# Performance work log

Measured on AMD Instinct MI355X. Metric: run time of the kernel, lower is better.

## Reference

```python
import jax, jax.numpy as jnp
import numpy as np

ANG = 5  # angRes; n = ANG*ANG
EPS = 1e-12  # torch F.normalize eps

def _l2norm(x, axis):
    n = jnp.sqrt(jnp.sum(x * x, axis=axis, keepdims=True))
    return x / jnp.maximum(n, EPS)

def setup_inputs() -> dict:
    key = jax.random.key(0)
    kq, kk, kv = jax.random.split(key, 3)
    shape = (16, 16, 25, 16, 128)  # b c n h w
    return {
        "token_q": jax.random.normal(kq, shape, dtype=jnp.float32),
        "token_k": jax.random.normal(kk, shape, dtype=jnp.float32),
        "token_v": jax.random.normal(kv, shape, dtype=jnp.float32),
    }

def reference(token_q, token_k, token_v):
    b, c, n, h, w = token_q.shape
    u = v = ANG
    buffer = token_v

    def to_q(x):  # b c (u v) h w -> b (c h) (w u v)
        return x.reshape(b, c, u, v, h, w).transpose(0, 1, 4, 5, 2, 3).reshape(b, c * h, w * u * v)

    def to_k(x):  # b c (u v) h w -> b (w u v) (c h)
        return x.reshape(b, c, u, v, h, w).transpose(0, 5, 2, 3, 1, 4).reshape(b, w * u * v, c * h)

    unfold_q = _l2norm(to_q(token_q), axis=-1)      # [b, ch, wuv]
    unfold_k = _l2norm(to_k(token_k), axis=-2)      # [b, wuv, ch]
    unfold_v = to_q(token_v)                        # [b, ch, wuv]

    att = jnp.einsum('bts,bsr->btr', unfold_q, unfold_k)  # [b, ch, ch]
    size = c * h
    causal = jnp.tril(jnp.ones((size, size), dtype=bool))
    att = jnp.where(causal, att, jnp.float32(-1e15))
    att = jax.nn.softmax(att, axis=-1)

    out = jnp.einsum('btr,brs->bts', att, unfold_v)  # [b, ch, wuv]
    # b (c h) (w u v) -> b c (u v) h w
    out = out.reshape(b, c, h, w, u, v).transpose(0, 1, 4, 5, 2, 3).reshape(b, c, n, h, w)
    return out + buffer
```

## Files before the change

kernel.cpp:

```cpp
#include <hip/hip_runtime.h>
#include <math.h>

#define SB 819200
#define SC 51200
#define SN 2048
#define CH 256
#define NW 3200
#define NPARTS 5
#define PARTLEN 640
#define SPART 1048576

typedef __bf16 bf16x8 __attribute__((ext_vector_type(8)));
typedef __bf16 bf16x4 __attribute__((ext_vector_type(4)));
typedef float  f32x4  __attribute__((ext_vector_type(4)));

__device__ __forceinline__ bf16x8 cvt8(float4 a, float4 b) {
    bf16x8 r;
    r[0] = (__bf16)a.x; r[1] = (__bf16)a.y; r[2] = (__bf16)a.z; r[3] = (__bf16)a.w;
    r[4] = (__bf16)b.x; r[5] = (__bf16)b.y; r[6] = (__bf16)b.z; r[7] = (__bf16)b.w;
    return r;
}

__global__ __launch_bounds__(256) void norms_kernel(const float* __restrict__ q,
                                                    const float* __restrict__ k,
                                                    float* __restrict__ inv_nq,
                                                    float* __restrict__ inv_nk) {
    const int wave = threadIdx.x >> 6;
    const int lane = threadIdx.x & 63;
    const int row = blockIdx.x * 4 + wave;
    const int b = row >> 8;
    const int t = row & 255;
    const size_t base = (size_t)b * SB + (size_t)(t >> 4) * SC +
                        (size_t)(t & 15) * 128 + lane * 2;
    float sq = 0.f, sk = 0.f;
#pragma unroll
    for (int nch = 0; nch < 25; nch++) {
        const float2 a = *(const float2*)(q + base + (size_t)nch * SN);
        const float2 c = *(const float2*)(k + base + (size_t)nch * SN);
        sq += a.x * a.x + a.y * a.y;
        sk += c.x * c.x + c.y * c.y;
    }
#pragma unroll
    for (int off = 32; off; off >>= 1) {
        sq += __shfl_xor(sq, off, 64);
        sk += __shfl_xor(sk, off, 64);
    }
    if (lane == 0) {
        inv_nq[row] = 1.0f / fmaxf(sqrtf(sq), 1e-12f);
        inv_nk[row] = 1.0f / fmaxf(sqrtf(sk), 1e-12f);
    }
}

__global__ __launch_bounds__(256, 2) void gemm1_kernel(const float* __restrict__ q,
                                                       const float* __restrict__ k,
                                                       float* __restrict__ Sp) {
    __shared__ alignas(16) __bf16 As[128 * 72];
    __shared__ alignas(16) __bf16 Bs[128 * 72];

    const int tid = threadIdx.x;
    const int b = blockIdx.z;
    const int part = blockIdx.y;
    const int tile = blockIdx.x;
    const int tm = (tile + 1) >> 1;
    const int tn = tile >> 1;

    const int lane = tid & 63;
    const int wave = tid >> 6;
    const int wm = wave >> 1;
    const int wn = wave & 1;

    const int srow = tid >> 1;
    const int scol = (tid & 1) * 32;
    const int ta = tm * 128 + srow;
    const int rb = tn * 128 + srow;
    const float* qrow = q + (size_t)b * SB + (size_t)(ta >> 4) * SC + (size_t)(ta & 15) * 128;
    const float* krow = k + (size_t)b * SB + (size_t)(rb >> 4) * SC + (size_t)(rb & 15) * 128;

    f32x4 acc[4][4] = {};
    bool live[4][4];
#pragma unroll
    for (int mi = 0; mi < 4; mi++)
#pragma unroll
        for (int ni = 0; ni < 4; ni++)
            live[mi][ni] = (tn * 128 + wn * 64 + ni * 16) <= (tm * 128 + wm * 64 + mi * 16);

    for (int ch = 0; ch < 10; ch++) {
        const int kg = part * PARTLEN + ch * 64;
        const size_t koff = (size_t)(kg >> 7) * SN + (kg & 127) + scol;

        float4 av[8], bv[8];
#pragma unroll
        for (int j = 0; j < 8; j++) {
            av[j] = *(const float4*)(qrow + koff + j * 4);
            bv[j] = *(const float4*)(krow + koff + j * 4);
        }
        __syncthreads();
#pragma unroll
        for (int j = 0; j < 4; j++) {
            *(bf16x8*)&As[srow * 72 + scol + j * 8] = cvt8(av[2 * j], av[2 * j + 1]);
            *(bf16x8*)&Bs[srow * 72 + scol + j * 8] = cvt8(bv[2 * j], bv[2 * j + 1]);
        }
        __syncthreads();
#pragma unroll
        for (int ks = 0; ks < 2; ks++) {
            const int ko = ks * 32 + (lane >> 4) * 8;
            bf16x8 af[4], bf[4];
#pragma unroll
            for (int mi = 0; mi < 4; mi++)
                af[mi] = *(const bf16x8*)&As[(wm * 64 + mi * 16 + (lane & 15)) * 72 + ko];
#pragma unroll
            for (int ni = 0; ni < 4; ni++)
                bf[ni] = *(const bf16x8*)&Bs[(wn * 64 + ni * 16 + (lane & 15)) * 72 + ko];
#pragma unroll
            for (int mi = 0; mi < 4; mi++)
#pragma unroll
                for (int ni = 0; ni < 4; ni++)
                    if (live[mi][ni])
                        acc[mi][ni] = __builtin_amdgcn_mfma_f32_16x16x32_bf16(
                            af[mi], bf[ni], acc[mi][ni], 0, 0, 0);
        }
    }

    float* o = Sp + (size_t)part * SPART + (size_t)b * 65536;
#pragma unroll
    for (int mi = 0; mi < 4; mi++)
#pragma unroll
        for (int ni = 0; ni < 4; ni++) {
            if (!live[mi][ni]) continue;
            const int r = tn * 128 + wn * 64 + ni * 16 + (lane & 15);
#pragma unroll
            for (int j = 0; j < 4; j++) {
                const int t = tm * 128 + wm * 64 + mi * 16 + (lane >> 4) * 4 + j;
                o[(size_t)t * 256 + r] = acc[mi][ni][j];
            }
        }
}

__global__ __launch_bounds__(256) void softmax_kernel(const float* __restrict__ Sp,
                                                      const float* __restrict__ inv_nq,
                                                      const float* __restrict__ inv_nk,
                                                      __bf16* __restrict__ P) {
    const int wave = threadIdx.x >> 6;
    const int lane = threadIdx.x & 63;
    const int t = blockIdx.x * 4 + wave;
    const int b = blockIdx.y;
    const size_t rowbase = ((size_t)b * 256 + t) * 256;
    const int r0 = lane * 4;

    float4 s4 = {0.f, 0.f, 0.f, 0.f};
#pragma unroll
    for (int p = 0; p < NPARTS; p++) {
        const float4 x = *(const float4*)(Sp + (size_t)p * SPART + rowbase + r0);
        s4.x += x.x; s4.y += x.y; s4.z += x.z; s4.w += x.w;
    }
    const float qn = inv_nq[b * 256 + t];
    const float4 kn = *(const float4*)(inv_nk + b * 256 + r0);

    float val[4] = {s4.x * qn * kn.x, s4.y * qn * kn.y,
                    s4.z * qn * kn.z, s4.w * qn * kn.w};
    float m = -1e30f;
#pragma unroll
    for (int j = 0; j < 4; j++) {
        if (r0 + j > t) val[j] = -1e30f;
        m = fmaxf(m, val[j]);
    }
#pragma unroll
    for (int off = 32; off; off >>= 1) m = fmaxf(m, __shfl_xor(m, off, 64));

    float e[4], sum = 0.f;
#pragma unroll
    for (int j = 0; j < 4; j++) {
        e[j] = (r0 + j <= t) ? expf(val[j] - m) : 0.f;
        sum += e[j];
    }
#pragma unroll
    for (int off = 32; off; off >>= 1) sum += __shfl_xor(sum, off, 64);

    const float inv = 1.0f / sum;
    bf16x4 o;
    o[0] = (__bf16)(e[0] * inv);
    o[1] = (__bf16)(e[1] * inv);
    o[2] = (__bf16)(e[2] * inv);
    o[3] = (__bf16)(e[3] * inv);
    *(bf16x4*)(P + rowbase + r0) = o;
}

__global__ __launch_bounds__(256, 4) void gemm2_kernel(const __bf16* __restrict__ P,
                                                       const float* __restrict__ v,
                                                       float* __restrict__ out) {
    __shared__ alignas(16) char smem[36864];
    __bf16* Ps = (__bf16*)smem;
    __bf16* Vs = (__bf16*)(smem + 18432);
    float* Es = (float*)smem;

    const int tid = threadIdx.x;
    const int b = blockIdx.z;
    const int tt = blockIdx.y;
    const int n = blockIdx.x;

    const int lane = tid & 63;
    const int wave = tid >> 6;
    const int wm = wave >> 1;
    const int wn = wave & 1;

    const int prow = tid >> 1;
    const int pcol = (tid & 1) * 32;
    const __bf16* Prow = P + ((size_t)b * 256 + tt * 128 + prow) * 256;

    const int vu = tid & 7;
    const int vr = tid >> 3;
    const float* vbase = v + (size_t)b * SB + (size_t)n * SN;

    f32x4 acc[4][4] = {};

    for (int kc = 0; kc < 4; kc++) {
        bf16x8 p4[4];
#pragma unroll
        for (int j = 0; j < 4; j++)
            p4[j] = *(const bf16x8*)(Prow + kc * 64 + pcol + j * 8);

        float4 vv[2][4];
#pragma unroll
        for (int g = 0; g < 2; g++) {
            const int rg = kc * 64 + vr + g * 32;
            const float* vrow = vbase + (size_t)(rg >> 4) * SC + (size_t)(rg & 15) * 128;
#pragma unroll
            for (int jj = 0; jj < 4; jj++)
                vv[g][jj] = *(const float4*)(vrow + vu * 16 + jj * 4);
        }
        __syncthreads();
#pragma unroll
        for (int j = 0; j < 4; j++)
            *(bf16x8*)&Ps[prow * 72 + pcol + j * 8] = p4[j];
#pragma unroll
        for (int g = 0; g < 2; g++) {
            const int rl = vr + g * 32;
            const int rsw = rl ^ (vu << 3);
#pragma unroll
            for (int jj = 0; jj < 4; jj++) {
                const float* f = (const float*)&vv[g][jj];
#pragma unroll
                for (int e = 0; e < 4; e++) {
                    const int s = vu * 16 + jj * 4 + e;
                    Vs[s * 72 + rsw] = (__bf16)f[e];
                }
            }
        }
        __syncthreads();
#pragma unroll
        for (int ks = 0; ks < 2; ks++) {
            const int ko = ks * 32 + (lane >> 4) * 8;
            bf16x8 af[4], bf[4];
#pragma unroll
            for (int mi = 0; mi < 4; mi++)
                af[mi] = *(const bf16x8*)&Ps[(wm * 64 + mi * 16 + (lane & 15)) * 72 + ko];
#pragma unroll
            for (int ni = 0; ni < 4; ni++) {
                const int s0 = wn * 64 + ni * 16;
                const int sw = ((s0 >> 4) & 7) << 3;
                bf[ni] = *(const bf16x8*)&Vs[(s0 + (lane & 15)) * 72 + (ko ^ sw)];
            }
#pragma unroll
            for (int mi = 0; mi < 4; mi++)
#pragma unroll
                for (int ni = 0; ni < 4; ni++)
                    acc[mi][ni] = __builtin_amdgcn_mfma_f32_16x16x32_bf16(
                        af[mi], bf[ni], acc[mi][ni], 0, 0, 0);
        }
        __syncthreads();
    }

    for (int half = 0; half < 2; half++) {
        if (half == 1) __syncthreads();
        if (wm == half) {
#pragma unroll
            for (int mi = 0; mi < 4; mi++)
#pragma unroll
                for (int ni = 0; ni < 4; ni++)
#pragma unroll
                    for (int j = 0; j < 4; j++) {
                        const int trow = mi * 16 + (lane >> 4) * 4 + j;
                        const int wcol = wn * 64 + ni * 16 + (lane & 15);
                        Es[trow * 132 + wcol] = acc[mi][ni][j];
                    }
        }
        __syncthreads();
#pragma unroll
        for (int it = 0; it < 8; it++) {
            const int tl = it * 8 + (tid >> 5);
            const int w4 = (tid & 31) * 4;
            const int t = tt * 128 + half * 64 + tl;
            const size_t a = (size_t)b * SB + (size_t)(t >> 4) * SC + (size_t)n * SN +
                             (size_t)(t & 15) * 128 + w4;
            float4 r4 = *(const float4*)&Es[tl * 132 + w4];
            const float4 buf = *(const float4*)(v + a);
            r4.x += buf.x; r4.y += buf.y; r4.z += buf.z; r4.w += buf.w;
            *(float4*)(out + a) = r4;
        }
    }
}

extern "C" void kernel_launch(void* const* d_in, const int* in_sizes, int n_in,
                              void* d_out, int out_size, void* d_ws, size_t ws_size,
                              hipStream_t stream) {
    const float* q = (const float*)d_in[0];
    const float* k = (const float*)d_in[1];
    const float* v = (const float*)d_in[2];
    float* out = (float*)d_out;

    float* ws = (float*)d_ws;
    float* inv_nq = ws;
    float* inv_nk = ws + 4096;
    __bf16* P = (__bf16*)(ws + 8192);

    float* Spart = out;

    norms_kernel<<<dim3(1024), dim3(256), 0, stream>>>(q, k, inv_nq, inv_nk);
    gemm1_kernel<<<dim3(3, NPARTS, 16), dim3(256), 0, stream>>>(q, k, Spart);
    softmax_kernel<<<dim3(64, 16), dim3(256), 0, stream>>>(Spart, inv_nq, inv_nk, P);
    gemm2_kernel<<<dim3(25, 2, 16), dim3(256), 0, stream>>>(P, v, out);
}
```

Baseline: 246.6 us.

## Fuse norms into gemm1 launch and split gemm2 into narrower W tiles

Result: faster. 227.2 us (-7.9%).

```diff
diff --git a/kernel.cpp b/kernel.cpp
--- a/kernel.cpp
+++ b/kernel.cpp
@@ -9,9 +9,11 @@
 #define NPARTS 5
 #define PARTLEN 640
 #define SPART 1048576
+#define G1BLOCKS 240
 
 typedef __bf16 bf16x8 __attribute__((ext_vector_type(8)));
 typedef __bf16 bf16x4 __attribute__((ext_vector_type(4)));
+typedef __bf16 bf16x2 __attribute__((ext_vector_type(2)));
 typedef float  f32x4  __attribute__((ext_vector_type(4)));
 
 __device__ __forceinline__ bf16x8 cvt8(float4 a, float4 b) {
@@ -21,51 +23,51 @@
     return r;
 }
 
-__global__ __launch_bounds__(256) void norms_kernel(const float* __restrict__ q,
-                                                    const float* __restrict__ k,
-                                                    float* __restrict__ inv_nq,
-                                                    float* __restrict__ inv_nk) {
-    const int wave = threadIdx.x >> 6;
-    const int lane = threadIdx.x & 63;
-    const int row = blockIdx.x * 4 + wave;
-    const int b = row >> 8;
-    const int t = row & 255;
-    const size_t base = (size_t)b * SB + (size_t)(t >> 4) * SC +
-                        (size_t)(t & 15) * 128 + lane * 2;
-    float sq = 0.f, sk = 0.f;
-#pragma unroll
-    for (int nch = 0; nch < 25; nch++) {
-        const float2 a = *(const float2*)(q + base + (size_t)nch * SN);
-        const float2 c = *(const float2*)(k + base + (size_t)nch * SN);
-        sq += a.x * a.x + a.y * a.y;
-        sk += c.x * c.x + c.y * c.y;
-    }
-#pragma unroll
-    for (int off = 32; off; off >>= 1) {
-        sq += __shfl_xor(sq, off, 64);
-        sk += __shfl_xor(sk, off, 64);
-    }
-    if (lane == 0) {
-        inv_nq[row] = 1.0f / fmaxf(sqrtf(sq), 1e-12f);
-        inv_nk[row] = 1.0f / fmaxf(sqrtf(sk), 1e-12f);
-    }
-}
-
-__global__ __launch_bounds__(256, 2) void gemm1_kernel(const float* __restrict__ q,
-                                                       const float* __restrict__ k,
-                                                       float* __restrict__ Sp) {
+__global__ __launch_bounds__(256, 2) void gemm1_norms_kernel(const float* __restrict__ q,
+                                                             const float* __restrict__ k,
+                                                             float* __restrict__ Sp,
+                                                             float* __restrict__ inv_nq,
+                                                             float* __restrict__ inv_nk) {
     __shared__ alignas(16) __bf16 As[128 * 72];
     __shared__ alignas(16) __bf16 Bs[128 * 72];
 
     const int tid = threadIdx.x;
-    const int b = blockIdx.z;
-    const int part = blockIdx.y;
-    const int tile = blockIdx.x;
+    const int lane = tid & 63;
+    const int wave = tid >> 6;
+
+    if (blockIdx.x >= G1BLOCKS) {
+        const int row = (blockIdx.x - G1BLOCKS) * 4 + wave;
+        const int b = row >> 8;
+        const int t = row & 255;
+        const size_t base = (size_t)b * SB + (size_t)(t >> 4) * SC +
+                            (size_t)(t & 15) * 128 + lane * 2;
+        float sq = 0.f, sk = 0.f;
+#pragma unroll
+        for (int nch = 0; nch < 25; nch++) {
+            const float2 a = *(const float2*)(q + base + (size_t)nch * SN);
+            const float2 c = *(const float2*)(k + base + (size_t)nch * SN);
+            sq += a.x * a.x + a.y * a.y;
+            sk += c.x * c.x + c.y * c.y;
+        }
+#pragma unroll
+        for (int off = 32; off; off >>= 1) {
+            sq += __shfl_xor(sq, off, 64);
+            sk += __shfl_xor(sk, off, 64);
+        }
+        if (lane == 0) {
+            inv_nq[row] = 1.0f / fmaxf(sqrtf(sq), 1e-12f);
+            inv_nk[row] = 1.0f / fmaxf(sqrtf(sk), 1e-12f);
+        }
+        return;
+    }
+
+    const int bx = blockIdx.x;
+    const int tile = bx % 3;
+    const int part = (bx / 3) % NPARTS;
+    const int b = bx / (3 * NPARTS);
     const int tm = (tile + 1) >> 1;
     const int tn = tile >> 1;
 
-    const int lane = tid & 63;
-    const int wave = tid >> 6;
     const int wm = wave >> 1;
     const int wn = wave & 1;
 
@@ -188,111 +190,105 @@
 __global__ __launch_bounds__(256, 4) void gemm2_kernel(const __bf16* __restrict__ P,
                                                        const float* __restrict__ v,
                                                        float* __restrict__ out) {
-    __shared__ alignas(16) char smem[36864];
-    __bf16* Ps = (__bf16*)smem;
-    __bf16* Vs = (__bf16*)(smem + 18432);
+    __shared__ alignas(16) char smem[9216];
+    __bf16* Vs = (__bf16*)smem;
     float* Es = (float*)smem;
 
     const int tid = threadIdx.x;
     const int b = blockIdx.z;
     const int tt = blockIdx.y;
-    const int n = blockIdx.x;
+    const int nw = blockIdx.x;
+    const int n = nw >> 1;
+    const int whalf = nw & 1;
 
     const int lane = tid & 63;
     const int wave = tid >> 6;
     const int wm = wave >> 1;
     const int wn = wave & 1;
-
-    const int prow = tid >> 1;
-    const int pcol = (tid & 1) * 32;
-    const __bf16* Prow = P + ((size_t)b * 256 + tt * 128 + prow) * 256;
+    const int l15 = lane & 15;
+    const int quad = lane >> 4;
 
     const int vu = tid & 7;
-    const int vr = tid >> 3;
-    const float* vbase = v + (size_t)b * SB + (size_t)n * SN;
-
-    f32x4 acc[4][4] = {};
+    const int rp = tid >> 3;
+    const float* vbase = v + (size_t)b * SB + (size_t)n * SN + whalf * 64;
+
+    const __bf16* Pbase = P + ((size_t)b * 256 + tt * 128 + wm * 64 + l15) * 256 + quad * 8;
+
+    f32x4 acc[4][2] = {};
 
     for (int kc = 0; kc < 4; kc++) {
-        bf16x8 p4[4];
-#pragma unroll
-        for (int j = 0; j < 4; j++)
-            p4[j] = *(const bf16x8*)(Prow + kc * 64 + pcol + j * 8);
-
-        float4 vv[2][4];
-#pragma unroll
-        for (int g = 0; g < 2; g++) {
-            const int rg = kc * 64 + vr + g * 32;
-            const float* vrow = vbase + (size_t)(rg >> 4) * SC + (size_t)(rg & 15) * 128;
-#pragma unroll
-            for (int jj = 0; jj < 4; jj++)
-                vv[g][jj] = *(const float4*)(vrow + vu * 16 + jj * 4);
-        }
-        __syncthreads();
-#pragma unroll
-        for (int j = 0; j < 4; j++)
-            *(bf16x8*)&Ps[prow * 72 + pcol + j * 8] = p4[j];
-#pragma unroll
-        for (int g = 0; g < 2; g++) {
-            const int rl = vr + g * 32;
-            const int rsw = rl ^ (vu << 3);
-#pragma unroll
-            for (int jj = 0; jj < 4; jj++) {
-                const float* f = (const float*)&vv[g][jj];
-#pragma unroll
-                for (int e = 0; e < 4; e++) {
-                    const int s = vu * 16 + jj * 4 + e;
-                    Vs[s * 72 + rsw] = (__bf16)f[e];
+        bf16x8 af[4][2];
+#pragma unroll
+        for (int mi = 0; mi < 4; mi++)
+#pragma unroll
+            for (int ks = 0; ks < 2; ks++)
+                af[mi][ks] = *(const bf16x8*)(Pbase + (size_t)mi * 16 * 256 + kc * 64 + ks * 32);
+
+        float vr0[8], vr1[8];
+        {
+            const int r0 = kc * 64 + 2 * rp;
+            const int r1 = r0 + 1;
+            const float* row0 = vbase + (size_t)(r0 >> 4) * SC + (size_t)(r0 & 15) * 128;
+            const float* row1 = vbase + (size_t)(r1 >> 4) * SC + (size_t)(r1 & 15) * 128;
+            *(float4*)&vr0[0] = *(const float4*)(row0 + vu * 8);
+            *(float4*)&vr0[4] = *(const float4*)(row0 + vu * 8 + 4);
+            *(float4*)&vr1[0] = *(const float4*)(row1 + vu * 8);
+            *(float4*)&vr1[4] = *(const float4*)(row1 + vu * 8 + 4);
+        }
+        __syncthreads();
+        {
+            const int rl0 = 2 * rp;
+#pragma unroll
+            for (int sj = 0; sj < 8; sj++) {
+                const int s = vu * 8 + sj;
+                bf16x2 pr;
+                pr[0] = (__bf16)vr0[sj];
+                pr[1] = (__bf16)vr1[sj];
+                *(bf16x2*)&Vs[s * 72 + (rl0 ^ (s & 0x38))] = pr;
+            }
+        }
+        __syncthreads();
+#pragma unroll
+        for (int ks = 0; ks < 2; ks++) {
+            bf16x8 bfr[2];
+#pragma unroll
+            for (int ni = 0; ni < 2; ni++) {
+                const int s = wn * 32 + ni * 16 + l15;
+                bfr[ni] = *(const bf16x8*)&Vs[s * 72 + ((ks * 32 + quad * 8) ^ (s & 0x38))];
+            }
+#pragma unroll
+            for (int mi = 0; mi < 4; mi++)
+#pragma unroll
+                for (int ni = 0; ni < 2; ni++)
+                    acc[mi][ni] = __builtin_amdgcn_mfma_f32_16x16x32_bf16(
+                        af[mi][ks], bfr[ni], acc[mi][ni], 0, 0, 0);
+        }
+    }
+
+    for (int p = 0; p < 4; p++) {
+        __syncthreads();
+        if (wm == (p >> 1)) {
+            const int mibase = (p & 1) * 2;
+#pragma unroll
+            for (int mm = 0; mm < 2; mm++)
+#pragma unroll
+                for (int ni = 0; ni < 2; ni++) {
+                    const f32x4 a = acc[mibase + mm][ni];
+                    const int wcol = wn * 32 + ni * 16 + l15;
+#pragma unroll
+                    for (int j = 0; j < 4; j++)
+                        Es[(mm * 16 + quad * 4 + j) * 68 + wcol] = a[j];
                 }
-            }
-        }
-        __syncthreads();
-#pragma unroll
-        for (int ks = 0; ks < 2; ks++) {
-            const int ko = ks * 32 + (lane >> 4) * 8;
-            bf16x8 af[4], bf[4];
-#pragma unroll
-            for (int mi = 0; mi < 4; mi++)
-                af[mi] = *(const bf16x8*)&Ps[(wm * 64 + mi * 16 + (lane & 15)) * 72 + ko];
-#pragma unroll
-            for (int ni = 0; ni < 4; ni++) {
-                const int s0 = wn * 64 + ni * 16;
-                const int sw = ((s0 >> 4) & 7) << 3;
-                bf[ni] = *(const bf16x8*)&Vs[(s0 + (lane & 15)) * 72 + (ko ^ sw)];
-            }
-#pragma unroll
-            for (int mi = 0; mi < 4; mi++)
-#pragma unroll
-                for (int ni = 0; ni < 4; ni++)
-                    acc[mi][ni] = __builtin_amdgcn_mfma_f32_16x16x32_bf16(
-                        af[mi], bf[ni], acc[mi][ni], 0, 0, 0);
-        }
-        __syncthreads();
-    }
-
-    for (int half = 0; half < 2; half++) {
-        if (half == 1) __syncthreads();
-        if (wm == half) {
-#pragma unroll
-            for (int mi = 0; mi < 4; mi++)
-#pragma unroll
-                for (int ni = 0; ni < 4; ni++)
-#pragma unroll
-                    for (int j = 0; j < 4; j++) {
-                        const int trow = mi * 16 + (lane >> 4) * 4 + j;
-                        const int wcol = wn * 64 + ni * 16 + (lane & 15);
-                        Es[trow * 132 + wcol] = acc[mi][ni][j];
-                    }
-        }
-        __syncthreads();
-#pragma unroll
-        for (int it = 0; it < 8; it++) {
-            const int tl = it * 8 + (tid >> 5);
-            const int w4 = (tid & 31) * 4;
-            const int t = tt * 128 + half * 64 + tl;
+        }
+        __syncthreads();
+#pragma unroll
+        for (int it = 0; it < 2; it++) {
+            const int tl = it * 16 + (tid >> 4);
+            const int w4 = (tid & 15) * 4;
+            const int t = tt * 128 + p * 32 + tl;
             const size_t a = (size_t)b * SB + (size_t)(t >> 4) * SC + (size_t)n * SN +
-                             (size_t)(t & 15) * 128 + w4;
-            float4 r4 = *(const float4*)&Es[tl * 132 + w4];
+                             (size_t)(t & 15) * 128 + whalf * 64 + w4;
+            float4 r4 = *(const float4*)&Es[tl * 68 + w4];
             const float4 buf = *(const float4*)(v + a);
             r4.x += buf.x; r4.y += buf.y; r4.z += buf.z; r4.w += buf.w;
             *(float4*)(out + a) = r4;
@@ -315,8 +311,8 @@
 
     float* Spart = out;
 
-    norms_kernel<<<dim3(1024), dim3(256), 0, stream>>>(q, k, inv_nq, inv_nk);
-    gemm1_kernel<<<dim3(3, NPARTS, 16), dim3(256), 0, stream>>>(q, k, Spart);
+    gemm1_norms_kernel<<<dim3(G1BLOCKS + 1024), dim3(256), 0, stream>>>(
+        q, k, Spart, inv_nq, inv_nk);
     softmax_kernel<<<dim3(64, 16), dim3(256), 0, stream>>>(Spart, inv_nq, inv_nk, P);
-    gemm2_kernel<<<dim3(25, 2, 16), dim3(256), 0, stream>>>(P, v, out);
-}
+    gemm2_kernel<<<dim3(50, 2, 16), dim3(256), 0, stream>>>(P, v, out);
+}
```
